# Kernel tuning notes

Hardware: AMD Instinct MI355X
Metric: run time of the kernel (lower is better)

Reference implementation:

```python
import jax, jax.numpy as jnp
import numpy as np

EPS = 1e-8
TEMPERATURE = 0.5


def setup_inputs() -> dict:
    key = jax.random.key(0)
    k1, k2, k3, k4 = jax.random.split(key, 4)
    B, DIN, DOUT = 4096, 2048, 128
    return {
        "zi": jax.random.normal(k1, (B, DIN), dtype=jnp.float32),
        "zj": jax.random.normal(k2, (B, DIN), dtype=jnp.float32),
        "W": jax.random.normal(k3, (DOUT, DIN), dtype=jnp.float32) * 0.02,
        "b": jax.random.normal(k4, (DOUT,), dtype=jnp.float32) * 0.02,
    }


def reference(zi, zj, W, b):
    # MLP projection head: Linear(ReLU(x))
    hi = jax.nn.relu(zi) @ W.T + b  # [B, 128]
    hj = jax.nn.relu(zj) @ W.T + b  # [B, 128]
    B = hi.shape[0]
    N = 2 * B
    reps = jnp.concatenate([hi, hj], axis=0)  # [2B, 128]
    # Cosine similarity: normalize once (torch eps=1e-8 clamp), then one matmul
    norms = jnp.maximum(jnp.linalg.norm(reps, axis=-1, keepdims=True), EPS)
    zn = reps / norms
    sim = (zn @ zn.T) / TEMPERATURE  # [2B, 2B]
    idx = jnp.arange(N)
    # positive pair index: i <-> i +/- B
    pos = sim[idx, (idx + B) % N]  # [2B]
    # denominator: all j != i (self excluded, positive included once) ==
    # torch's [positive, negatives(mask excludes diag and +/-B diags)] logits
    NEG_INF = jnp.asarray(-1e9, sim.dtype)
    sim_masked = jnp.where(idx[:, None] == idx[None, :], NEG_INF, sim)
    lse = jax.scipy.special.logsumexp(sim_masked, axis=1)  # [2B]
    loss = jnp.mean(lse - pos)
    return loss
```

## Files before the change

kernel.cpp:

```cpp
#include <hip/hip_runtime.h>
#include <math.h>

#define DIN    2048
#define DOUT   128
#define BHALF  4096
#define NTOT   8192
#define NSPLIT 16
#define JSPAN  512

typedef __bf16 bf16x8 __attribute__((ext_vector_type(8)));
typedef float  f32x4  __attribute__((ext_vector_type(4)));
typedef unsigned int u32x4 __attribute__((ext_vector_type(4)));

#define MFMA16 __builtin_amdgcn_mfma_f32_16x16x32_bf16

struct PackedPair { unsigned int h, l; };

__device__ __forceinline__ unsigned int bf16_rne(float f) {
    unsigned int u = __float_as_uint(f);
    return (u + 0x7fffu + ((u >> 16) & 1u)) >> 16;
}
__device__ __forceinline__ float bf16f(unsigned int h) {
    return __uint_as_float(h << 16);
}
__device__ __forceinline__ PackedPair split2(float a, float b) {
    unsigned int h0 = bf16_rne(a), h1 = bf16_rne(b);
    unsigned int g0 = bf16_rne(a - bf16f(h0)), g1 = bf16_rne(b - bf16f(h1));
    PackedPair r;
    r.h = h0 | (h1 << 16);
    r.l = g0 | (g1 << 16);
    return r;
}


__global__ __launch_bounds__(256) void wsplit_kernel(
    const float* __restrict__ W,
    unsigned short* __restrict__ Whp, unsigned short* __restrict__ Wlp,
    float* __restrict__ out)
{
    int t = blockIdx.x * 256 + threadIdx.x;
    if (t == 0) out[0] = 0.f;
    int l  = t & 63;
    int ks = (t >> 6) & 63;
    int g  = t >> 12;
    int c  = g * 16 + (l & 15);
    int k0 = ks * 32 + ((l >> 4) << 3);
    const float* src = W + (size_t)c * DIN + k0;
    f32x4 v0 = *(const f32x4*)src;
    f32x4 v1 = *(const f32x4*)(src + 4);
    u32x4 hv, lv;
    PackedPair p0 = split2(v0[0], v0[1]);  hv[0] = p0.h; lv[0] = p0.l;
    PackedPair p1 = split2(v0[2], v0[3]);  hv[1] = p1.h; lv[1] = p1.l;
    PackedPair p2 = split2(v1[0], v1[1]);  hv[2] = p2.h; lv[2] = p2.l;
    PackedPair p3 = split2(v1[2], v1[3]);  hv[3] = p3.h; lv[3] = p3.l;
    size_t off = ((size_t)(g * 64 + ks) * 64 + l) * 8;
    *(u32x4*)(Whp + off) = hv;
    *(u32x4*)(Wlp + off) = lv;
}

__global__ __launch_bounds__(512, 4) void proj_kernel(
    const float* __restrict__ zi, const float* __restrict__ zj,
    const unsigned short* __restrict__ Whp, const unsigned short* __restrict__ Wlp,
    const float* __restrict__ bvec,
    unsigned short* __restrict__ Zhp, unsigned short* __restrict__ Zlp)
{
    __shared__ float Red[4][16][132];
    const int t = threadIdx.x;
    const int w = t >> 6;
    const int lane = t & 63;
    const int r15 = lane & 15, q = lane >> 4;
    const int row0 = blockIdx.x * 16;
    const float* zsrc = (row0 < BHALF) ? zi : zj;
    const int zr0 = (row0 < BHALF) ? row0 : row0 - BHALF;

    f32x4 acc[8];
    #pragma unroll
    for (int g = 0; g < 8; g++) acc[g] = (f32x4){0.f, 0.f, 0.f, 0.f};

    const float* zrow = zsrc + (size_t)(zr0 + r15) * DIN + q * 8;
    f32x4 pv0 = *(const f32x4*)(zrow + w * 256);
    f32x4 pv1 = *(const f32x4*)(zrow + w * 256 + 4);

    #pragma unroll
    for (int i = 0; i < 8; i++) {
        const int ks = w * 8 + i;
        f32x4 v0 = pv0, v1 = pv1;
        if (i < 7) {
            pv0 = *(const f32x4*)(zrow + w * 256 + (i + 1) * 32);
            pv1 = *(const f32x4*)(zrow + w * 256 + (i + 1) * 32 + 4);
        }
        #pragma unroll
        for (int p = 0; p < 4; p++) {
            v0[p] = fmaxf(v0[p], 0.f);
            v1[p] = fmaxf(v1[p], 0.f);
        }
        u32x4 hv, lv;
        PackedPair p0 = split2(v0[0], v0[1]);  hv[0] = p0.h; lv[0] = p0.l;
        PackedPair p1 = split2(v0[2], v0[3]);  hv[1] = p1.h; lv[1] = p1.l;
        PackedPair p2 = split2(v1[0], v1[1]);  hv[2] = p2.h; lv[2] = p2.l;
        PackedPair p3 = split2(v1[2], v1[3]);  hv[3] = p3.h; lv[3] = p3.l;
        bf16x8 ah = __builtin_bit_cast(bf16x8, hv);
        bf16x8 al = __builtin_bit_cast(bf16x8, lv);
        #pragma unroll
        for (int g = 0; g < 8; g++) {
            size_t bo = ((size_t)(g * 64 + ks) * 64 + lane) * 8;
            bf16x8 bh = __builtin_bit_cast(bf16x8, *(const u32x4*)(Whp + bo));
            bf16x8 bl = __builtin_bit_cast(bf16x8, *(const u32x4*)(Wlp + bo));
            acc[g] = MFMA16(ah, bh, acc[g], 0, 0, 0);
            acc[g] = MFMA16(ah, bl, acc[g], 0, 0, 0);
            acc[g] = MFMA16(al, bh, acc[g], 0, 0, 0);
        }
    }

    if (w >= 4) {
        #pragma unroll
        for (int g = 0; g < 8; g++)
            #pragma unroll
            for (int r = 0; r < 4; r++)
                Red[w - 4][q * 4 + r][g * 16 + r15] = acc[g][r];
    }
    __syncthreads();
    if (w < 4) {
        #pragma unroll
        for (int g = 0; g < 8; g++)
            #pragma unroll
            for (int r = 0; r < 4; r++)
                Red[w][q * 4 + r][g * 16 + r15] += acc[g][r];
    }
    __syncthreads();

    const int row = t >> 5;
    const int tx  = t & 31;
    float v[4];
    #pragma unroll
    for (int j = 0; j < 4; j++) {
        v[j] = Red[0][row][tx * 4 + j] + Red[1][row][tx * 4 + j]
             + Red[2][row][tx * 4 + j] + Red[3][row][tx * 4 + j];
    }
    const f32x4 bb = *(const f32x4*)(bvec + tx * 4);
    v[0] += bb[0]; v[1] += bb[1]; v[2] += bb[2]; v[3] += bb[3];
    float ssq = v[0]*v[0] + v[1]*v[1] + v[2]*v[2] + v[3]*v[3];
    #pragma unroll
    for (int msk = 1; msk < 32; msk <<= 1) ssq += __shfl_xor(ssq, msk);
    const float inv = 1.f / fmaxf(sqrtf(ssq), 1e-8f);
    const int grow = row0 + row;
    const int gg = grow >> 4, rr = grow & 15;
    #pragma unroll
    for (int j = 0; j < 4; j++) {
        const int k = tx * 4 + j;
        float x = v[j] * inv;
        unsigned int h  = bf16_rne(x);
        unsigned int lo = bf16_rne(x - bf16f(h));
        size_t off = (((size_t)gg * 4 + (k >> 5)) * 64
                      + (rr | (((k >> 3) & 3) << 4))) * 8 + (k & 7);
        Zhp[off] = (unsigned short)h;
        Zlp[off] = (unsigned short)lo;
    }
}

__global__ __launch_bounds__(256, 4) void sim_kernel(
    const unsigned short* __restrict__ Zhp, const unsigned short* __restrict__ Zlp,
    float* __restrict__ Spart, float* __restrict__ P)
{
    __shared__ unsigned short Jt[16384];
    const int t = threadIdx.x;
    const int w = t >> 6, lane = t & 63;
    const int r15 = lane & 15, rq = lane >> 4;
    const int iblk   = blockIdx.x >> 4;
    const int jsplit = blockIdx.x & 15;
    const int rowbase = iblk * 128 + w * 32;

    bf16x8 Ah[2][4], Al[2][4];
    #pragma unroll
    for (int m = 0; m < 2; m++) {
        const int gA = iblk * 8 + w * 2 + m;
        #pragma unroll
        for (int ks = 0; ks < 4; ks++) {
            size_t ao = (((size_t)gA * 4 + ks) * 64 + lane) * 8;
            Ah[m][ks] = __builtin_bit_cast(bf16x8, *(const u32x4*)(Zhp + ao));
            Al[m][ks] = __builtin_bit_cast(bf16x8, *(const u32x4*)(Zlp + ao));
        }
    }

    float rs[2][4], ps[2][4];
    #pragma unroll
    for (int m = 0; m < 2; m++)
        #pragma unroll
        for (int r = 0; r < 4; r++) { rs[m][r] = 0.f; ps[m][r] = 0.f; }

    for (int jt = 0; jt < JSPAN / 64; jt++) {
        const int j0 = jsplit * JSPAN + jt * 64;
        __syncthreads();
        #pragma unroll
        for (int rr = 0; rr < 8; rr++) {
            const int cid = rr * 4 + w;
            const int hl = cid >> 4, jg = (cid >> 2) & 3, ks = cid & 3;
            const unsigned short* src = hl ? Zlp : Zhp;
            const unsigned short* gp = src
                + (((size_t)((j0 >> 4) + jg) * 4 + ks) * 64 + lane) * 8;
            unsigned short* lp = &Jt[(size_t)(rr * 256 + w * 64) * 8];
            __builtin_amdgcn_global_load_lds(
                (const __attribute__((address_space(1))) unsigned int*)gp,
                (__attribute__((address_space(3))) unsigned int*)lp, 16, 0, 0);
        }
        __syncthreads();

        f32x4 acc[2][4];
        #pragma unroll
        for (int m = 0; m < 2; m++)
            #pragma unroll
            for (int jg = 0; jg < 4; jg++) acc[m][jg] = (f32x4){0.f,0.f,0.f,0.f};

        #pragma unroll
        for (int ks = 0; ks < 4; ks++) {
            #pragma unroll
            for (int jg = 0; jg < 4; jg++) {
                bf16x8 bh = __builtin_bit_cast(bf16x8,
                    *(const u32x4*)&Jt[((jg * 4 + ks) * 64 + lane) * 8]);
                bf16x8 bl = __builtin_bit_cast(bf16x8,
                    *(const u32x4*)&Jt[((jg * 4 + ks + 16) * 64 + lane) * 8]);
                #pragma unroll
                for (int m = 0; m < 2; m++) {
                    acc[m][jg] = MFMA16(Ah[m][ks], bh, acc[m][jg], 0, 0, 0);
                    acc[m][jg] = MFMA16(Ah[m][ks], bl, acc[m][jg], 0, 0, 0);
                    acc[m][jg] = MFMA16(Al[m][ks], bh, acc[m][jg], 0, 0, 0);
                }
            }
        }

        #pragma unroll
        for (int m = 0; m < 2; m++) {
            const int growb = rowbase + m * 16 + rq * 4;
            #pragma unroll
            for (int jg = 0; jg < 4; jg++) {
                const int gcol = j0 + jg * 16 + r15;
                #pragma unroll
                for (int r = 0; r < 4; r++) {
                    float s = 2.f * acc[m][jg][r];
                    const int grow = growb + r;
                    float e = __expf(s);
                    if (gcol == grow) e = 0.f;
                    rs[m][r] += e;
                    if (gcol == (grow ^ BHALF)) ps[m][r] += s;
                }
            }
        }
    }

    #pragma unroll
    for (int m = 0; m < 2; m++)
        #pragma unroll
        for (int r = 0; r < 4; r++) {
            float a = rs[m][r], p = ps[m][r];
            #pragma unroll
            for (int msk = 1; msk < 16; msk <<= 1) {
                a += __shfl_xor(a, msk);
                p += __shfl_xor(p, msk);
            }
            if (r15 == 0) {
                const int grow = rowbase + m * 16 + rq * 4 + r;
                Spart[jsplit * NTOT + grow] = a;
                if (((grow ^ BHALF) >> 9) == jsplit) P[grow] = p;
            }
        }
}

__global__ __launch_bounds__(256) void loss_kernel(
    const float* __restrict__ Spart, const float* __restrict__ P,
    float* __restrict__ out)
{
    const int i = blockIdx.x * 256 + threadIdx.x;
    float ssum = 0.f;
    #pragma unroll
    for (int sp = 0; sp < NSPLIT; sp++) ssum += Spart[sp * NTOT + i];
    float v = logf(ssum) - P[i];
    #pragma unroll
    for (int msk = 1; msk < 64; msk <<= 1) v += __shfl_xor(v, msk);
    __shared__ float red[4];
    if ((threadIdx.x & 63) == 0) red[threadIdx.x >> 6] = v;
    __syncthreads();
    if (threadIdx.x == 0)
        atomicAdd(out, (red[0] + red[1] + red[2] + red[3]) * (1.f / (float)NTOT));
}

extern "C" void kernel_launch(void* const* d_in, const int* in_sizes, int n_in,
                              void* d_out, int out_size, void* d_ws, size_t ws_size,
                              hipStream_t stream) {
    const float* zi = (const float*)d_in[0];
    const float* zj = (const float*)d_in[1];
    const float* W  = (const float*)d_in[2];
    const float* bv = (const float*)d_in[3];
    float* out = (float*)d_out;

    char* ws = (char*)d_ws;
    unsigned short* Whp = (unsigned short*)(ws);
    unsigned short* Wlp = (unsigned short*)(ws + (512 << 10));
    unsigned short* Zhp = (unsigned short*)(ws + (1024 << 10));
    unsigned short* Zlp = (unsigned short*)(ws + (3072 << 10));
    float* Spart = (float*)(ws);
    float* P     = (float*)(ws + (512 << 10));

    wsplit_kernel<<<128, 256, 0, stream>>>(W, Whp, Wlp, out);
    proj_kernel<<<512, 512, 0, stream>>>(zi, zj, Whp, Wlp, bv, Zhp, Zlp);
    sim_kernel<<<1024, 256, 0, stream>>>(Zhp, Zlp, Spart, P);
    loss_kernel<<<NTOT / 256, 256, 0, stream>>>(Spart, P, out);
}
```

Measured before the change: 198.5 us.

## Double-buffer J tiles in sim kernel and halve the column splits

```diff
diff --git a/kernel.cpp b/kernel.cpp
--- a/kernel.cpp
+++ b/kernel.cpp
@@ -5,8 +5,8 @@
 #define DOUT   128
 #define BHALF  4096
 #define NTOT   8192
-#define NSPLIT 16
-#define JSPAN  512
+#define NSPLIT 8
+#define JSPAN  1024
 
 typedef __bf16 bf16x8 __attribute__((ext_vector_type(8)));
 typedef float  f32x4  __attribute__((ext_vector_type(4)));
@@ -158,17 +158,36 @@
     }
 }
 
-__global__ __launch_bounds__(256, 4) void sim_kernel(
+__global__ __launch_bounds__(256, 2) void sim_kernel(
     const unsigned short* __restrict__ Zhp, const unsigned short* __restrict__ Zlp,
     float* __restrict__ Spart, float* __restrict__ P)
 {
-    __shared__ unsigned short Jt[16384];
+    __shared__ unsigned short Jt[2][16384];
     const int t = threadIdx.x;
     const int w = t >> 6, lane = t & 63;
     const int r15 = lane & 15, rq = lane >> 4;
-    const int iblk   = blockIdx.x >> 4;
-    const int jsplit = blockIdx.x & 15;
+    const int jsplit = blockIdx.x & 7;
+    const int iblk   = blockIdx.x >> 3;
     const int rowbase = iblk * 128 + w * 32;
+    const int j0base  = jsplit * JSPAN;
+
+#define STAGE(jt_, buf_) do {                                                 \
+        const int jref_ = (j0base >> 4) + (jt_) * 4;                          \
+        _Pragma("unroll")                                                     \
+        for (int rr_ = 0; rr_ < 8; rr_++) {                                   \
+            const int cid_ = rr_ * 4 + w;                                     \
+            const int hl_ = cid_ >> 4, jg_ = (cid_ >> 2) & 3, ks_ = cid_ & 3; \
+            const unsigned short* src_ = hl_ ? Zlp : Zhp;                     \
+            const unsigned short* gp_ = src_ +                                \
+                (((size_t)(jref_ + jg_) * 4 + ks_) * 64 + lane) * 8;          \
+            unsigned short* lp_ = &Jt[buf_][(cid_ * 64) * 8];                 \
+            __builtin_amdgcn_global_load_lds(                                 \
+                (const __attribute__((address_space(1))) unsigned int*)gp_,   \
+                (__attribute__((address_space(3))) unsigned int*)lp_,         \
+                16, 0, 0);                                                    \
+        } } while (0)
+
+    STAGE(0, 0);
 
     bf16x8 Ah[2][4], Al[2][4];
     #pragma unroll
@@ -188,23 +207,20 @@
         #pragma unroll
         for (int r = 0; r < 4; r++) { rs[m][r] = 0.f; ps[m][r] = 0.f; }
 
-    for (int jt = 0; jt < JSPAN / 64; jt++) {
-        const int j0 = jsplit * JSPAN + jt * 64;
-        __syncthreads();
-        #pragma unroll
-        for (int rr = 0; rr < 8; rr++) {
-            const int cid = rr * 4 + w;
-            const int hl = cid >> 4, jg = (cid >> 2) & 3, ks = cid & 3;
-            const unsigned short* src = hl ? Zlp : Zhp;
-            const unsigned short* gp = src
-                + (((size_t)((j0 >> 4) + jg) * 4 + ks) * 64 + lane) * 8;
-            unsigned short* lp = &Jt[(size_t)(rr * 256 + w * 64) * 8];
-            __builtin_amdgcn_global_load_lds(
-                (const __attribute__((address_space(1))) unsigned int*)gp,
-                (__attribute__((address_space(3))) unsigned int*)lp, 16, 0, 0);
-        }
-        __syncthreads();
-
+    #pragma unroll 2
+    for (int jt = 0; jt < 16; jt++) {
+        const int cur = jt & 1;
+        const int j0 = j0base + jt * 64;
+        if (jt < 15) {
+            STAGE(jt + 1, cur ^ 1);
+            asm volatile("s_waitcnt vmcnt(8)" ::: "memory");
+        } else {
+            asm volatile("s_waitcnt vmcnt(0)" ::: "memory");
+        }
+        __builtin_amdgcn_s_barrier();
+        __builtin_amdgcn_sched_barrier(0);
+
+        const unsigned short* J = &Jt[cur][0];
         f32x4 acc[2][4];
         #pragma unroll
         for (int m = 0; m < 2; m++)
@@ -216,9 +232,9 @@
             #pragma unroll
             for (int jg = 0; jg < 4; jg++) {
                 bf16x8 bh = __builtin_bit_cast(bf16x8,
-                    *(const u32x4*)&Jt[((jg * 4 + ks) * 64 + lane) * 8]);
+                    *(const u32x4*)&J[((jg * 4 + ks) * 64 + lane) * 8]);
                 bf16x8 bl = __builtin_bit_cast(bf16x8,
-                    *(const u32x4*)&Jt[((jg * 4 + ks + 16) * 64 + lane) * 8]);
+                    *(const u32x4*)&J[((jg * 4 + ks + 16) * 64 + lane) * 8]);
                 #pragma unroll
                 for (int m = 0; m < 2; m++) {
                     acc[m][jg] = MFMA16(Ah[m][ks], bh, acc[m][jg], 0, 0, 0);
@@ -230,22 +246,32 @@
 
         #pragma unroll
         for (int m = 0; m < 2; m++) {
-            const int growb = rowbase + m * 16 + rq * 4;
+            const int rb16 = rowbase + m * 16;
             #pragma unroll
             for (int jg = 0; jg < 4; jg++) {
-                const int gcol = j0 + jg * 16 + r15;
-                #pragma unroll
-                for (int r = 0; r < 4; r++) {
-                    float s = 2.f * acc[m][jg][r];
-                    const int grow = growb + r;
-                    float e = __expf(s);
-                    if (gcol == grow) e = 0.f;
-                    rs[m][r] += e;
-                    if (gcol == (grow ^ BHALF)) ps[m][r] += s;
+                const int cb16 = j0 + jg * 16;
+                if (cb16 != rb16 && cb16 != (rb16 ^ BHALF)) {
+                    #pragma unroll
+                    for (int r = 0; r < 4; r++)
+                        rs[m][r] += __expf(2.f * acc[m][jg][r]);
+                } else {
+                    const int gcol = cb16 + r15;
+                    #pragma unroll
+                    for (int r = 0; r < 4; r++) {
+                        float s = 2.f * acc[m][jg][r];
+                        const int grow = rb16 + rq * 4 + r;
+                        float e = __expf(s);
+                        if (gcol == grow) e = 0.f;
+                        rs[m][r] += e;
+                        if (gcol == (grow ^ BHALF)) ps[m][r] += s;
+                    }
                 }
             }
         }
-    }
+        __builtin_amdgcn_sched_barrier(0);
+        __builtin_amdgcn_s_barrier();
+    }
+#undef STAGE
 
     #pragma unroll
     for (int m = 0; m < 2; m++)
@@ -260,7 +286,7 @@
             if (r15 == 0) {
                 const int grow = rowbase + m * 16 + rq * 4 + r;
                 Spart[jsplit * NTOT + grow] = a;
-                if (((grow ^ BHALF) >> 9) == jsplit) P[grow] = p;
+                if (((grow ^ BHALF) >> 10) == jsplit) P[grow] = p;
             }
         }
 }
@@ -298,10 +324,10 @@
     unsigned short* Zhp = (unsigned short*)(ws + (1024 << 10));
     unsigned short* Zlp = (unsigned short*)(ws + (3072 << 10));
     float* Spart = (float*)(ws);
-    float* P     = (float*)(ws + (512 << 10));
+    float* P     = (float*)(ws + (256 << 10));
 
     wsplit_kernel<<<128, 256, 0, stream>>>(W, Whp, Wlp, out);
     proj_kernel<<<512, 512, 0, stream>>>(zi, zj, Whp, Wlp, bv, Zhp, Zlp);
-    sim_kernel<<<1024, 256, 0, stream>>>(Zhp, Zlp, Spart, P);
+    sim_kernel<<<512, 256, 0, stream>>>(Zhp, Zlp, Spart, P);
     loss_kernel<<<NTOT / 256, 256, 0, stream>>>(Spart, P, out);
 }
```

After: 171.2 us. 1.16x faster.
